# Kernel tuning notes

Hardware: AMD Instinct MI355X
Metric: run time of the kernel (lower is better)

The kernel has to match this reference:

```python
import jax, jax.numpy as jnp
import numpy as np

B, S, D_IN, D_QK, D_V = 4, 4096, 1024, 64, 64

def setup_inputs() -> dict:
    key = jax.random.key(0)
    ks = jax.random.split(key, 8)
    sd = 1.0 / np.sqrt(D_IN)
    return {
        "X": jax.random.normal(ks[0], (B, S, D_IN), dtype=jnp.float32),
        "mask": jnp.ones((B, S, 1), dtype=jnp.float32),
        "Wq": jax.random.uniform(ks[1], (D_IN, D_QK), jnp.float32, -sd, sd),
        "bq": jax.random.uniform(ks[2], (D_QK,), jnp.float32, -sd, sd),
        "Wk": jax.random.uniform(ks[3], (D_IN, D_QK), jnp.float32, -sd, sd),
        "bk": jax.random.uniform(ks[4], (D_QK,), jnp.float32, -sd, sd),
        "Wv": jax.random.uniform(ks[5], (D_IN, D_V), jnp.float32, -sd, sd),
        "bv": jax.random.uniform(ks[6], (D_V,), jnp.float32, -sd, sd),
    }

def reference(X, mask, Wq, bq, Wk, bk, Wv, bv):
    # ReLU-activated projections (no head split, no 1/sqrt(d) scaling)
    q = jax.nn.relu(jnp.einsum('bsd,df->bsf', X, Wq) + bq)   # [B,S,D_QK]
    k = jax.nn.relu(jnp.einsum('bsd,df->bsf', X, Wk) + bk)   # [B,S,D_QK]
    v = jax.nn.relu(jnp.einsum('bsd,df->bsf', X, Wv) + bv)   # [B,S,D_V]
    scores = jax.nn.softmax(jnp.einsum('bqf,bkf->bqk', q, k), axis=-1)  # [B,S,S]
    return jnp.einsum('bqk,bkf->bqf', scores, v) * mask       # mask applied AFTER AV
```

## Files before the change

### kernel.cpp

```cpp
#include <hip/hip_runtime.h>


typedef short s16x8 __attribute__((ext_vector_type(8)));
typedef float fx4   __attribute__((ext_vector_type(4)));
typedef unsigned short u16x4 __attribute__((ext_vector_type(4)));

#define LOG2E 1.4426950408889634f

__device__ __forceinline__ unsigned short f2bf(float x) {
    unsigned int u = __float_as_uint(x);
    u += 0x7FFFu + ((u >> 16) & 1u);
    return (unsigned short)(u >> 16);
}
__device__ __forceinline__ float bf2f(unsigned short b) {
    return __uint_as_float(((unsigned int)b) << 16);
}

__global__ __launch_bounds__(256) void prep_w_kernel(
    const float* __restrict__ Wq, const float* __restrict__ Wk, const float* __restrict__ Wv,
    unsigned short* __restrict__ wt_hi, unsigned short* __restrict__ wt_lo)
{
    int idx = blockIdx.x * 256 + threadIdx.x;
    int y = idx >> 16;
    int r = idx & 65535;
    int k = r >> 6;
    int c = r & 63;
    const float* W = (y == 0) ? Wq : (y == 1) ? Wk : Wv;
    float x = W[r];
    unsigned short h = f2bf(x);
    unsigned short l = f2bf(x - bf2f(h));
    int o = (y * 64 + c) * 1024 + k;
    wt_hi[o] = h; wt_lo[o] = l;
}

__global__ __launch_bounds__(512, 6) void proj_kernel(
    const float* __restrict__ X,
    const unsigned short* __restrict__ wt_hi, const unsigned short* __restrict__ wt_lo,
    const float* __restrict__ bq, const float* __restrict__ bk, const float* __restrict__ bv,
    unsigned short* __restrict__ q_hi, unsigned short* __restrict__ q_lo,
    unsigned short* __restrict__ k_bf, unsigned short* __restrict__ vt_g)
{
    __shared__ __align__(16) unsigned short a_buf[2][64][72];
    __shared__ __align__(16) unsigned short b_hi[64][72];
    __shared__ __align__(16) unsigned short b_lo[64][72];

    const int tid  = threadIdx.x;
    const int lane = tid & 63;
    const int w    = tid >> 6;
    const int quad = lane >> 4;
    const int l15  = lane & 15;
    const int rs   = w & 3;
    const int ch   = w >> 2;
    const int y    = blockIdx.x;
    const int m0   = blockIdx.y * 64;

    fx4 acc[2];
    acc[0] = (fx4){0.f, 0.f, 0.f, 0.f};
    acc[1] = (fx4){0.f, 0.f, 0.f, 0.f};

    const int xrow = tid >> 4;
    const int xoff = (tid & 15) * 4;
    const int wrow = tid >> 3;
    const int woff = (tid & 7) * 8;

    fx4   xr[2];
    s16x8 wrh, wrl;
    #pragma unroll
    for (int i = 0; i < 2; i++)
        xr[i] = *(const fx4*)(X + (size_t)(m0 + xrow + i * 32) * 1024 + xoff);
    {
        size_t g = (size_t)(y * 64 + wrow) * 1024 + woff;
        wrh = *(const s16x8*)(wt_hi + g);
        wrl = *(const s16x8*)(wt_lo + g);
    }

    for (int kc = 0; kc < 16; kc++) {
        if (kc) __syncthreads();
        #pragma unroll
        for (int i = 0; i < 2; i++) {
            fx4 xv = xr[i];
            unsigned short h0 = f2bf(xv.x), h1 = f2bf(xv.y), h2 = f2bf(xv.z), h3 = f2bf(xv.w);
            unsigned short l0 = f2bf(xv.x - bf2f(h0)), l1 = f2bf(xv.y - bf2f(h1));
            unsigned short l2 = f2bf(xv.z - bf2f(h2)), l3 = f2bf(xv.w - bf2f(h3));
            *(u16x4*)&a_buf[0][xrow + i * 32][xoff] = (u16x4){h0, h1, h2, h3};
            *(u16x4*)&a_buf[1][xrow + i * 32][xoff] = (u16x4){l0, l1, l2, l3};
        }
        *(s16x8*)&b_hi[wrow][woff] = wrh;
        *(s16x8*)&b_lo[wrow][woff] = wrl;
        __syncthreads();

        if (kc < 15) {
            #pragma unroll
            for (int i = 0; i < 2; i++)
                xr[i] = *(const fx4*)(X + (size_t)(m0 + xrow + i * 32) * 1024 + (kc + 1) * 64 + xoff);
            size_t g = (size_t)(y * 64 + wrow) * 1024 + (kc + 1) * 64 + woff;
            wrh = *(const s16x8*)(wt_hi + g);
            wrl = *(const s16x8*)(wt_lo + g);
        }

        s16x8 ah[2], al[2];
        #pragma unroll
        for (int ks = 0; ks < 2; ks++) {
            int r = rs * 16 + l15;
            ah[ks] = *(const s16x8*)&a_buf[0][r][ks * 32 + quad * 8];
            al[ks] = *(const s16x8*)&a_buf[1][r][ks * 32 + quad * 8];
        }
        #pragma unroll
        for (int nt = 0; nt < 2; nt++) {
            #pragma unroll
            for (int ks = 0; ks < 2; ks++) {
                s16x8 bh = *(const s16x8*)&b_hi[ch * 32 + nt * 16 + l15][ks * 32 + quad * 8];
                s16x8 bl = *(const s16x8*)&b_lo[ch * 32 + nt * 16 + l15][ks * 32 + quad * 8];
                acc[nt] = __builtin_amdgcn_mfma_f32_16x16x32_bf16(ah[ks], bh, acc[nt], 0, 0, 0);
                acc[nt] = __builtin_amdgcn_mfma_f32_16x16x32_bf16(ah[ks], bl, acc[nt], 0, 0, 0);
                acc[nt] = __builtin_amdgcn_mfma_f32_16x16x32_bf16(al[ks], bh, acc[nt], 0, 0, 0);
            }
        }
    }
    __syncthreads();

    const float* bias = (y == 0) ? bq : (y == 1) ? bk : bv;
    const int b   = m0 >> 12;
    const int s0b = m0 & 4095;
    unsigned short* vtr = &a_buf[0][0][0];

    #pragma unroll
    for (int nt = 0; nt < 2; nt++) {
        int col = ch * 32 + nt * 16 + l15;
        float bb = bias[col];
        int rloc = rs * 16 + quad * 4;
        #pragma unroll
        for (int r = 0; r < 4; r++) {
            float v = acc[nt][r] + bb;
            v = fmaxf(v, 0.f);
            size_t grow = (size_t)(m0 + rloc + r);
            if (y == 0) {
                unsigned short h = f2bf(v);
                unsigned short l = f2bf(v - bf2f(h));
                q_hi[grow * 64 + col] = h;
                q_lo[grow * 64 + col] = l;
            } else if (y == 1) {
                k_bf[grow * 64 + col] = f2bf(v);
            } else {
                vtr[col * 72 + rloc + r] = f2bf(v);
            }
        }
    }
    if (y == 2) {
        __syncthreads();
        int row = tid >> 3;
        int off = (tid & 7) * 8;
        s16x8 vv = *(const s16x8*)&vtr[row * 72 + off];
        *(s16x8*)(vt_g + (size_t)(b * 64 + row) * 4096 + s0b + off) = vv;
    }
}

__global__ __launch_bounds__(256, 6) void attn_kernel(
    const unsigned short* __restrict__ q_hi, const unsigned short* __restrict__ q_lo,
    const unsigned short* __restrict__ k_bf, const unsigned short* __restrict__ vt_g,
    unsigned short* __restrict__ pOb, float* __restrict__ pL)
{
    __shared__ __align__(16) unsigned short kt[64][72];
    __shared__ __align__(16) unsigned short vt[64][72];
    __shared__ __align__(16) unsigned short pt[4][16][40];

    const int tid  = threadIdx.x;
    const int lane = tid & 63;
    const int w    = tid >> 6;
    const int quad = lane >> 4;
    const int l15  = lane & 15;
    const int ck   = blockIdx.y;
    const int b    = blockIdx.z;
    const int q0   = blockIdx.x * 64;

    const size_t qoff = ((size_t)b * 4096 + q0 + w * 16 + l15) * 64 + quad * 8;
    s16x8 qh0 = *(const s16x8*)(q_hi + qoff);
    s16x8 qh1 = *(const s16x8*)(q_hi + qoff + 32);
    s16x8 ql0 = *(const s16x8*)(q_lo + qoff);
    s16x8 ql1 = *(const s16x8*)(q_lo + qoff + 32);

    fx4 accO[4];
    #pragma unroll
    for (int nt = 0; nt < 4; nt++) accO[nt] = (fx4){0.f, 0.f, 0.f, 0.f};
    float lsum[4] = {0.f, 0.f, 0.f, 0.f};

    const unsigned short* kgb = k_bf + (size_t)b * 4096 * 64;
    const unsigned short* vgb = vt_g + (size_t)b * 64 * 4096;

    const int srow = tid >> 3;
    const int soff = (tid & 7) * 8;

    for (int it = ck * 8; it < ck * 8 + 8; it++) {
        const unsigned short* kg = kgb + (size_t)it * 4096;
        #pragma unroll
        for (int i = 0; i < 2; i++) {
            int row = srow + i * 32;
            *(s16x8*)&kt[row][soff] = *(const s16x8*)(kg + (size_t)row * 64 + soff);
            *(s16x8*)&vt[row][soff] = *(const s16x8*)(vgb + (size_t)row * 4096 + it * 64 + soff);
        }
        __syncthreads();

        #pragma unroll
        for (int kh = 0; kh < 2; kh++) {
            #pragma unroll
            for (int nt2 = 0; nt2 < 2; nt2++) {
                int key = kh * 32 + nt2 * 16 + l15;
                s16x8 k0 = *(const s16x8*)&kt[key][quad * 8];
                s16x8 k1 = *(const s16x8*)&kt[key][32 + quad * 8];
                fx4 sc = (fx4){0.f, 0.f, 0.f, 0.f};
                sc = __builtin_amdgcn_mfma_f32_16x16x32_bf16(qh0, k0, sc, 0, 0, 0);
                sc = __builtin_amdgcn_mfma_f32_16x16x32_bf16(ql0, k0, sc, 0, 0, 0);
                sc = __builtin_amdgcn_mfma_f32_16x16x32_bf16(qh1, k1, sc, 0, 0, 0);
                sc = __builtin_amdgcn_mfma_f32_16x16x32_bf16(ql1, k1, sc, 0, 0, 0);
                #pragma unroll
                for (int r = 0; r < 4; r++) {
                    float p = __builtin_amdgcn_exp2f(sc[r] * LOG2E);
                    unsigned short pb = f2bf(p);
                    lsum[r] += bf2f(pb);
                    pt[w][quad * 4 + r][nt2 * 16 + l15] = pb;
                }
            }
            s16x8 pa = *(const s16x8*)&pt[w][l15][quad * 8];
            #pragma unroll
            for (int nt = 0; nt < 4; nt++) {
                s16x8 vf = *(const s16x8*)&vt[nt * 16 + l15][kh * 32 + quad * 8];
                accO[nt] = __builtin_amdgcn_mfma_f32_16x16x32_bf16(pa, vf, accO[nt], 0, 0, 0);
            }
        }
        __syncthreads();
    }

    #pragma unroll
    for (int r = 0; r < 4; r++) {
        float v = lsum[r];
        #pragma unroll
        for (int o = 1; o < 16; o <<= 1) v += __shfl_xor(v, o);
        lsum[r] = v;
    }
    #pragma unroll
    for (int r = 0; r < 4; r++) {
        int qrow = q0 + w * 16 + quad * 4 + r;
        size_t grow = (size_t)b * 4096 + qrow;
        #pragma unroll
        for (int nt = 0; nt < 4; nt++)
            pOb[((size_t)ck * 16384 + grow) * 64 + nt * 16 + l15] = f2bf(accO[nt][r]);
        if (l15 == 0)
            pL[(size_t)ck * 16384 + grow] = lsum[r];
    }
}

__global__ __launch_bounds__(256) void combine_kernel(
    const unsigned short* __restrict__ pOb, const float* __restrict__ pL,
    const float* __restrict__ mask, float* __restrict__ out)
{
    int idx = blockIdx.x * 256 + threadIdx.x;
    int q  = idx >> 4;
    int dg = idx & 15;
    fx4 s = (fx4){0.f, 0.f, 0.f, 0.f};
    float l = 0.f;
    #pragma unroll
    for (int c = 0; c < 8; c++) {
        u16x4 h = *(const u16x4*)(pOb + ((size_t)c * 16384 + q) * 64 + dg * 4);
        s.x += bf2f(h.x);
        s.y += bf2f(h.y);
        s.z += bf2f(h.z);
        s.w += bf2f(h.w);
        l += pL[(size_t)c * 16384 + q];
    }
    float scale = mask[q] / l;
    *(fx4*)(out + (size_t)q * 64 + dg * 4) = s * scale;
}

extern "C" void kernel_launch(void* const* d_in, const int* in_sizes, int n_in,
                              void* d_out, int out_size, void* d_ws, size_t ws_size,
                              hipStream_t stream)
{
    const float* X    = (const float*)d_in[0];
    const float* mask = (const float*)d_in[1];
    const float* Wq   = (const float*)d_in[2];
    const float* bq   = (const float*)d_in[3];
    const float* Wk   = (const float*)d_in[4];
    const float* bk   = (const float*)d_in[5];
    const float* Wv   = (const float*)d_in[6];
    const float* bv   = (const float*)d_in[7];
    float* out = (float*)d_out;

    char* ws = (char*)d_ws;
    unsigned short* q_hi  = (unsigned short*)(ws);
    unsigned short* q_lo  = (unsigned short*)(ws + (size_t)(2u << 20));
    unsigned short* k_bf  = (unsigned short*)(ws + (size_t)(4u << 20));
    unsigned short* vt_g  = (unsigned short*)(ws + (size_t)(6u << 20));
    unsigned short* wt_hi = (unsigned short*)(ws + (size_t)(8u << 20));
    unsigned short* wt_lo = (unsigned short*)(ws + (size_t)(8u << 20) + 393216);
    unsigned short* pOb   = (unsigned short*)(ws + (size_t)(9u << 20));
    float*          pL    = (float*)(ws + (size_t)(25u << 20));

    hipLaunchKernelGGL(prep_w_kernel, dim3(768), dim3(256), 0, stream,
                       Wq, Wk, Wv, wt_hi, wt_lo);
    hipLaunchKernelGGL(proj_kernel, dim3(3, 256), dim3(512), 0, stream,
                       X, wt_hi, wt_lo, bq, bk, bv, q_hi, q_lo, k_bf, vt_g);
    hipLaunchKernelGGL(attn_kernel, dim3(64, 8, 4), dim3(256), 0, stream,
                       q_hi, q_lo, k_bf, vt_g, pOb, pL);
    hipLaunchKernelGGL(combine_kernel, dim3(1024), dim3(256), 0, stream,
                       pOb, pL, mask, out);
}
```

Before: 177.6 us.

## Tile weight transpose through LDS, deepen projection prefetch, remap blocks per XCD

The weight prep kernel now transposes 64x64 tiles through shared memory, so both its reads and its 16-byte writes are coalesced instead of scattered 2-byte stores. The projection kernel prefetches X four k-chunks ahead and the weights two chunks ahead, with occupancy hint lowered from 6 to 4 to make room for the extra registers. It also uses a flat 1D grid that places the three projections of the same row tile on the same XCD, so X is shared in that XCD's L2. The cost is higher register pressure and fewer resident waves.

```diff
diff --git a/kernel.cpp b/kernel.cpp
--- a/kernel.cpp
+++ b/kernel.cpp
@@ -20,20 +20,41 @@
     const float* __restrict__ Wq, const float* __restrict__ Wk, const float* __restrict__ Wv,
     unsigned short* __restrict__ wt_hi, unsigned short* __restrict__ wt_lo)
 {
-    int idx = blockIdx.x * 256 + threadIdx.x;
-    int y = idx >> 16;
-    int r = idx & 65535;
-    int k = r >> 6;
-    int c = r & 63;
+    __shared__ __align__(16) unsigned short sh[64][72];
+    __shared__ __align__(16) unsigned short sl[64][72];
+
+    const int y  = blockIdx.x;
+    const int kt = blockIdx.y;
     const float* W = (y == 0) ? Wq : (y == 1) ? Wk : Wv;
-    float x = W[r];
-    unsigned short h = f2bf(x);
-    unsigned short l = f2bf(x - bf2f(h));
-    int o = (y * 64 + c) * 1024 + k;
-    wt_hi[o] = h; wt_lo[o] = l;
-}
-
-__global__ __launch_bounds__(512, 6) void proj_kernel(
+    const int t  = threadIdx.x;
+
+    const int kl = t >> 2;
+    const int c0 = (t & 3) * 16;
+    const float* src = W + (size_t)(kt * 64 + kl) * 64 + c0;
+    #pragma unroll
+    for (int j = 0; j < 4; j++) {
+        fx4 v = *(const fx4*)(src + j * 4);
+        #pragma unroll
+        for (int i = 0; i < 4; i++) {
+            float x = v[i];
+            unsigned short h = f2bf(x);
+            unsigned short l = f2bf(x - bf2f(h));
+            sh[c0 + j * 4 + i][kl] = h;
+            sl[c0 + j * 4 + i][kl] = l;
+        }
+    }
+    __syncthreads();
+
+    const int c  = t >> 2;
+    const int k0 = (t & 3) * 16;
+    size_t o = (size_t)(y * 64 + c) * 1024 + kt * 64 + k0;
+    *(s16x8*)(wt_hi + o)     = *(const s16x8*)&sh[c][k0];
+    *(s16x8*)(wt_hi + o + 8) = *(const s16x8*)&sh[c][k0 + 8];
+    *(s16x8*)(wt_lo + o)     = *(const s16x8*)&sl[c][k0];
+    *(s16x8*)(wt_lo + o + 8) = *(const s16x8*)&sl[c][k0 + 8];
+}
+
+__global__ __launch_bounds__(512, 4) void proj_kernel(
     const float* __restrict__ X,
     const unsigned short* __restrict__ wt_hi, const unsigned short* __restrict__ wt_lo,
     const float* __restrict__ bq, const float* __restrict__ bk, const float* __restrict__ bv,
@@ -51,8 +72,12 @@
     const int l15  = lane & 15;
     const int rs   = w & 3;
     const int ch   = w >> 2;
-    const int y    = blockIdx.x;
-    const int m0   = blockIdx.y * 64;
+
+    const int f   = blockIdx.x;
+    const int xcd = f & 7;
+    const int jj  = f >> 3;
+    const int y   = jj % 3;
+    const int m0  = ((jj / 3) * 8 + xcd) * 64;
 
     fx4 acc[2];
     acc[0] = (fx4){0.f, 0.f, 0.f, 0.f};
@@ -63,39 +88,46 @@
     const int wrow = tid >> 3;
     const int woff = (tid & 7) * 8;
 
-    fx4   xr[2];
-    s16x8 wrh, wrl;
-    #pragma unroll
-    for (int i = 0; i < 2; i++)
-        xr[i] = *(const fx4*)(X + (size_t)(m0 + xrow + i * 32) * 1024 + xoff);
-    {
-        size_t g = (size_t)(y * 64 + wrow) * 1024 + woff;
-        wrh = *(const s16x8*)(wt_hi + g);
-        wrl = *(const s16x8*)(wt_lo + g);
-    }
-
+    const float* xb0 = X + (size_t)(m0 + xrow) * 1024 + xoff;
+    const float* xb1 = X + (size_t)(m0 + xrow + 32) * 1024 + xoff;
+    const size_t wb  = (size_t)(y * 64 + wrow) * 1024 + woff;
+
+    fx4   xr[4][2];
+    s16x8 wrh[2], wrl[2];
+    #pragma unroll
+    for (int d = 0; d < 4; d++) {
+        xr[d][0] = *(const fx4*)(xb0 + d * 64);
+        xr[d][1] = *(const fx4*)(xb1 + d * 64);
+    }
+    #pragma unroll
+    for (int d = 0; d < 2; d++) {
+        wrh[d] = *(const s16x8*)(wt_hi + wb + d * 64);
+        wrl[d] = *(const s16x8*)(wt_lo + wb + d * 64);
+    }
+
+    #pragma unroll 4
     for (int kc = 0; kc < 16; kc++) {
         if (kc) __syncthreads();
         #pragma unroll
         for (int i = 0; i < 2; i++) {
-            fx4 xv = xr[i];
+            fx4 xv = xr[kc & 3][i];
             unsigned short h0 = f2bf(xv.x), h1 = f2bf(xv.y), h2 = f2bf(xv.z), h3 = f2bf(xv.w);
             unsigned short l0 = f2bf(xv.x - bf2f(h0)), l1 = f2bf(xv.y - bf2f(h1));
             unsigned short l2 = f2bf(xv.z - bf2f(h2)), l3 = f2bf(xv.w - bf2f(h3));
             *(u16x4*)&a_buf[0][xrow + i * 32][xoff] = (u16x4){h0, h1, h2, h3};
             *(u16x4*)&a_buf[1][xrow + i * 32][xoff] = (u16x4){l0, l1, l2, l3};
         }
-        *(s16x8*)&b_hi[wrow][woff] = wrh;
-        *(s16x8*)&b_lo[wrow][woff] = wrl;
+        *(s16x8*)&b_hi[wrow][woff] = wrh[kc & 1];
+        *(s16x8*)&b_lo[wrow][woff] = wrl[kc & 1];
         __syncthreads();
 
-        if (kc < 15) {
-            #pragma unroll
-            for (int i = 0; i < 2; i++)
-                xr[i] = *(const fx4*)(X + (size_t)(m0 + xrow + i * 32) * 1024 + (kc + 1) * 64 + xoff);
-            size_t g = (size_t)(y * 64 + wrow) * 1024 + (kc + 1) * 64 + woff;
-            wrh = *(const s16x8*)(wt_hi + g);
-            wrl = *(const s16x8*)(wt_lo + g);
+        if (kc < 12) {
+            xr[kc & 3][0] = *(const fx4*)(xb0 + (kc + 4) * 64);
+            xr[kc & 3][1] = *(const fx4*)(xb1 + (kc + 4) * 64);
+        }
+        if (kc < 14) {
+            wrh[kc & 1] = *(const s16x8*)(wt_hi + wb + (kc + 2) * 64);
+            wrl[kc & 1] = *(const s16x8*)(wt_lo + wb + (kc + 2) * 64);
         }
 
         s16x8 ah[2], al[2];
@@ -295,9 +327,9 @@
     unsigned short* pOb   = (unsigned short*)(ws + (size_t)(9u << 20));
     float*          pL    = (float*)(ws + (size_t)(25u << 20));
 
-    hipLaunchKernelGGL(prep_w_kernel, dim3(768), dim3(256), 0, stream,
+    hipLaunchKernelGGL(prep_w_kernel, dim3(3, 16), dim3(256), 0, stream,
                        Wq, Wk, Wv, wt_hi, wt_lo);
-    hipLaunchKernelGGL(proj_kernel, dim3(3, 256), dim3(512), 0, stream,
+    hipLaunchKernelGGL(proj_kernel, dim3(768), dim3(512), 0, stream,
                        X, wt_hi, wt_lo, bq, bk, bv, q_hi, q_lo, k_bf, vt_g);
     hipLaunchKernelGGL(attn_kernel, dim3(64, 8, 4), dim3(256), 0, stream,
                        q_hi, q_lo, k_bf, vt_g, pOb, pL);
```

Measured after the change: 175.2 us. About the same (-1.3%).
